# Performance work log

Measured on AMD Instinct MI355X. Metric: run time of the kernel, lower is better.

The kernel has to match this reference:

```python
import jax, jax.numpy as jnp
import numpy as np

N = 100000      # number of nodes/edges
R = 32          # relation_dim
I = 256         # input_dim
O = 256         # output_dim


def setup_inputs() -> dict:
    key = jax.random.key(0)
    k1, k2, k3, k4 = jax.random.split(key, 4)
    x = jax.random.normal(k1, (N, I), dtype=jnp.float32)
    # relation weights per node (e.g. soft relation assignment), non-negative
    edge_attr = jax.random.uniform(k2, (N, R), dtype=jnp.float32)
    # xavier_uniform-style init for W [R, O, I] and b [R, O]
    a_w = float(np.sqrt(6.0 / (I + O)))
    W = jax.random.uniform(k3, (R, O, I), dtype=jnp.float32, minval=-a_w, maxval=a_w)
    a_b = float(np.sqrt(6.0 / (R + O)))
    b = jax.random.uniform(k4, (R, O), dtype=jnp.float32, minval=-a_b, maxval=a_b)
    return {"x": x, "edge_attr": edge_attr, "W": W, "b": b}


def reference(x, edge_attr, W, b):
    # y[n,o] = sum_r edge_attr[n,r] * (W[r] @ x[n])[o] + (edge_attr @ b)[n,o]
    # Stream over the small relation axis, accumulating into [N, O];
    # avoids materializing the naive [N, R, O] intermediate.
    def body(acc, s):
        W_r, e_r = s                      # W_r: [O, I], e_r: [N]
        acc = acc + e_r[:, None] * (x @ W_r.T)  # [N, O]
        return acc, None

    y0 = edge_attr @ b                    # bias term: [N, R] @ [R, O] -> [N, O]
    y, _ = jax.lax.scan(body, y0, (W, edge_attr.T))
    return y
```

## Files before the change

kernel.cpp:

```cpp
#include <hip/hip_runtime.h>
#include <hip/hip_bf16.h>


typedef __attribute__((ext_vector_type(4))) float f32x4;
typedef __attribute__((ext_vector_type(8))) short short8;
typedef __attribute__((ext_vector_type(8))) unsigned short ushort8;

#define R_DIM 32
#define I_DIM 256
#define O_DIM 256
#define KW    8192
#define KEXT  8256
#define BM    128
#define BN    256
#define BK    64
#define NT    (KEXT / BK)
#define NTHR  512

__device__ __forceinline__ unsigned short f2bf(float f) {
  unsigned u = __builtin_bit_cast(unsigned, f);
  u += 0x7FFFu + ((u >> 16) & 1u);
  return (unsigned short)(u >> 16);
}

__device__ __forceinline__ unsigned pk2(float a, float b) {
  __hip_bfloat162 h = __float22bfloat162_rn(make_float2(a, b));
  unsigned u;
  __builtin_memcpy(&u, &h, sizeof(u));
  return u;
}

__device__ __forceinline__ void gld_lds16(const void* g, void* l) {
  __builtin_amdgcn_global_load_lds(
      (const __attribute__((address_space(1))) unsigned int*)g,
      (__attribute__((address_space(3))) unsigned int*)l, 16, 0, 0);
}

__global__ void prep_w(const float* __restrict__ W, const float* __restrict__ b,
                       unsigned short* __restrict__ Wb) {
  const int id = blockIdx.x * 256 + threadIdx.x;
  const int o  = id / (KEXT / 4);
  const int k4 = (id - o * (KEXT / 4)) * 4;
  float v[4];
  if (k4 < KW) {
    const int r  = k4 & 31;
    const int ih = (k4 >> 5) & 1;
    const int il = k4 >> 6;
    const int i  = 128 * ih + il;
#pragma unroll
    for (int j = 0; j < 4; ++j)
      v[j] = W[((size_t)((r + j) * O_DIM + o)) * I_DIM + i];
  } else {
    const int kk = k4 - KW;
#pragma unroll
    for (int j = 0; j < 4; ++j)
      v[j] = (kk + j < R_DIM) ? b[(kk + j) * O_DIM + o] : 0.f;
  }
  uint2 pk;
  pk.x = pk2(v[0], v[1]);
  pk.y = pk2(v[2], v[3]);
  *(uint2*)&Wb[(size_t)o * KEXT + k4] = pk;
}

__global__ __launch_bounds__(NTHR)
__attribute__((amdgpu_waves_per_eu(2, 2)))
void lkg2p(
    const float* __restrict__ x, const float* __restrict__ e,
    const unsigned short* __restrict__ Wb, float* __restrict__ out, int Ntot) {
  __shared__ unsigned short Al[2][BM * BK];
  __shared__ unsigned short Bl[3][BN * BK];

  const int tid  = threadIdx.x;
  const int lane = tid & 63;
  const int w    = tid >> 6;
  const int wr   = w >> 2;
  const int wc   = w & 3;
  const int l15  = lane & 15;
  const int sx   = (l15 & 7) << 4;
  const int kb0  = (lane >> 4) << 4;

  const int m0   = (int)blockIdx.x * BM;
  const int srow = tid >> 2;
  const int q    = tid & 3;
  const int ih   = q >> 1;
  const int gr   = min(m0 + srow, Ntot - 1);

  const int bro = lane >> 3;
  const int bch = (lane & 7) ^ bro;

  float er[16];
#pragma unroll
  for (int p = 0; p < 4; ++p) {
    const float4 ev = *(const float4*)&e[(size_t)gr * R_DIM + (q & 1) * 16 + p * 4];
    er[p * 4 + 0] = ev.x; er[p * 4 + 1] = ev.y;
    er[p * 4 + 2] = ev.z; er[p * 4 + 3] = ev.w;
  }
  const float* xrow = x + (size_t)gr * I_DIM + ih * 128;
  const float bx = (ih == 0) ? 1.f : 0.f;

  f32x4 acc[4][4];
#pragma unroll
  for (int a = 0; a < 4; ++a)
#pragma unroll
    for (int c = 0; c < 4; ++c) acc[a][c] = (f32x4){0.f, 0.f, 0.f, 0.f};

  auto issueB4 = [&](unsigned short* Bd, int t2) {
    const size_t k0 = (size_t)t2 * BK;
#pragma unroll
    for (int g = 0; g < 4; ++g)
      gld_lds16(Wb + (size_t)(w * 32 + g * 8 + bro) * KEXT + k0 + bch * 8,
                Bd + (w * 32 + g * 8) * BK);
  };
  auto stageA = [&](unsigned short* Ad, float xs) {
    char* rowp = (char*)(Ad + srow * BK);
    const int sw = (srow & 7) << 4;
    const int qb = q * 32;
    uint4 wv;
    wv.x = pk2(xs * er[0], xs * er[1]);
    wv.y = pk2(xs * er[2], xs * er[3]);
    wv.z = pk2(xs * er[4], xs * er[5]);
    wv.w = pk2(xs * er[6], xs * er[7]);
    *(uint4*)(rowp + ((qb + 0) ^ sw)) = wv;
    uint4 wv2;
    wv2.x = pk2(xs * er[8],  xs * er[9]);
    wv2.y = pk2(xs * er[10], xs * er[11]);
    wv2.z = pk2(xs * er[12], xs * er[13]);
    wv2.w = pk2(xs * er[14], xs * er[15]);
    *(uint4*)(rowp + ((qb + 16) ^ sw)) = wv2;
  };
  auto rdA = [&](const unsigned short* Ab, int ks, int fr) -> short8 {
    const int row = wr * 64 + fr * 16 + l15;
    return *(const short8*)((const char*)Ab + row * 128 + ((ks * 64 + kb0) ^ sx));
  };
  auto rdB = [&](const unsigned short* Bb, int ks, int fc) -> short8 {
    const int row = wc * 64 + fc * 16 + l15;
    return *(const short8*)((const char*)Bb + row * 128 + ((ks * 64 + kb0) ^ sx));
  };

  auto tileF = [&](int t, float xs, int mode, int apar, int cb) {
    const unsigned short* Ac = Al[apar];
    unsigned short*       Aw = Al[apar ^ 1];
    const unsigned short* Bc = Bl[cb];
    unsigned short*       Bw = Bl[cb >= 1 ? cb - 1 : 2];

    short8 af[4], bf[4];

#pragma unroll
    for (int fr = 0; fr < 4; ++fr) af[fr] = rdA(Ac, 0, fr);
#pragma unroll
    for (int fc = 0; fc < 4; ++fc) bf[fc] = rdB(Bc, 0, fc);
    if (mode & 2) issueB4(Bw, t + 2);
    __builtin_amdgcn_s_barrier();
    asm volatile("s_waitcnt lgkmcnt(0)" ::: "memory");
    __builtin_amdgcn_s_setprio(1);
#pragma unroll
    for (int fr = 0; fr < 4; ++fr)
#pragma unroll
      for (int fc = 0; fc < 4; ++fc)
        acc[fr][fc] = __builtin_amdgcn_mfma_f32_16x16x32_bf16(af[fr], bf[fc],
                                                              acc[fr][fc], 0, 0, 0);
    __builtin_amdgcn_s_setprio(0);
    __builtin_amdgcn_s_barrier();

#pragma unroll
    for (int fr = 0; fr < 4; ++fr) af[fr] = rdA(Ac, 1, fr);
#pragma unroll
    for (int fc = 0; fc < 4; ++fc) bf[fc] = rdB(Bc, 1, fc);
    if (mode & 1) stageA(Aw, xs);
    asm volatile("s_waitcnt lgkmcnt(0)" ::: "memory");
    if (mode & 2) {
      asm volatile("s_waitcnt vmcnt(4)" ::: "memory");
    } else {
      asm volatile("s_waitcnt vmcnt(0)" ::: "memory");
    }
    __builtin_amdgcn_s_barrier();
    __builtin_amdgcn_s_setprio(1);
#pragma unroll
    for (int fr = 0; fr < 4; ++fr)
#pragma unroll
      for (int fc = 0; fc < 4; ++fc)
        acc[fr][fc] = __builtin_amdgcn_mfma_f32_16x16x32_bf16(af[fr], bf[fc],
                                                              acc[fr][fc], 0, 0, 0);
    __builtin_amdgcn_s_setprio(0);
    __builtin_amdgcn_s_barrier();
  };

  float4 xv = *(const float4*)xrow;
  stageA(Al[0], xv.x);
  issueB4(Bl[0], 0);
  issueB4(Bl[1], 1);
  asm volatile("s_waitcnt lgkmcnt(0)" ::: "memory");
  asm volatile("s_waitcnt vmcnt(4)" ::: "memory");
  __builtin_amdgcn_s_barrier();

  int cb = 0;
  for (int u = 0; u < 32; ++u) {
    float4 xvn = xv;
    if (u < 31) xvn = *(const float4*)(xrow + (u + 1) * 4);
    const int t0 = u * 4;
    tileF(t0 + 0, xv.y, 3, 0, cb); cb = (cb == 2) ? 0 : cb + 1;
    tileF(t0 + 1, xv.z, 3, 1, cb); cb = (cb == 2) ? 0 : cb + 1;
    tileF(t0 + 2, xv.w, 3, 0, cb); cb = (cb == 2) ? 0 : cb + 1;
    if (u < 31) {
      tileF(t0 + 3, xvn.x, 3, 1, cb);
    } else {
      tileF(t0 + 3, bx, 1, 1, cb);
    }
    cb = (cb == 2) ? 0 : cb + 1;
    xv = xvn;
  }
  tileF(128, 0.f, 0, 0, cb);

#pragma unroll
  for (int fr = 0; fr < 4; ++fr) {
    const int r0 = m0 + wr * 64 + fr * 16 + (lane >> 4) * 4;
#pragma unroll
    for (int j = 0; j < 4; ++j) {
      const int rr = r0 + j;
      if (rr < Ntot) {
#pragma unroll
        for (int fc = 0; fc < 4; ++fc) {
          const int col = wc * 64 + fc * 16 + l15;
          out[(size_t)rr * O_DIM + col] = acc[fr][fc][j];
        }
      }
    }
  }
}

__global__ __launch_bounds__(256) void lkg_fb(
    const float* __restrict__ x, const float* __restrict__ e,
    const float* __restrict__ Wf, const float* __restrict__ bf32,
    float* __restrict__ out, int Ntot) {
  const int FBK = 64;
  const int FNT = (KW + 64) / FBK;
  __shared__ unsigned short Alds[128 * 64];
  __shared__ unsigned short Blds[256 * 64];

  const int tid = threadIdx.x, lane = tid & 63, wid = tid >> 6;
  const int wr = wid >> 1, wc = wid & 1, l15 = lane & 15, lk8 = (lane >> 4) * 8;
  const int m0 = (int)blockIdx.x * 128;
  const int srow = tid >> 1, skq = (tid & 1) * 32;
  const int gr = min(m0 + srow, Ntot - 1);

  f32x4 acc[4][8];
#pragma unroll
  for (int a = 0; a < 4; ++a)
#pragma unroll
    for (int c = 0; c < 8; ++c) acc[a][c] = (f32x4){0.f, 0.f, 0.f, 0.f};

  for (int t = 0; t < FNT; ++t) {
    const int k0 = t * FBK;
    float av[32];
    if (k0 < KW) {
      const int r = k0 >> 8, i0 = k0 & 255;
      const float ev = e[(size_t)gr * R_DIM + r];
#pragma unroll
      for (int p = 0; p < 8; ++p) {
        const float4 xvv = *(const float4*)&x[(size_t)gr * I_DIM + i0 + skq + p * 4];
        av[p * 4 + 0] = xvv.x * ev; av[p * 4 + 1] = xvv.y * ev;
        av[p * 4 + 2] = xvv.z * ev; av[p * 4 + 3] = xvv.w * ev;
      }
    } else {
#pragma unroll
      for (int s2 = 0; s2 < 32; ++s2) {
        const int kk = skq + s2;
        av[s2] = (kk < R_DIM) ? e[(size_t)gr * R_DIM + kk] : 0.f;
      }
    }
    const int bo = tid;
    if (k0 < KW) {
      const int r = k0 >> 8, i0 = k0 & 255;
#pragma unroll
      for (int h = 0; h < 4; ++h) {
        float bv[16];
#pragma unroll
        for (int p = 0; p < 4; ++p) {
          const float4 wv =
              *(const float4*)&Wf[((size_t)(r * O_DIM + bo)) * I_DIM + i0 + h * 16 + p * 4];
          bv[p * 4 + 0] = wv.x; bv[p * 4 + 1] = wv.y;
          bv[p * 4 + 2] = wv.z; bv[p * 4 + 3] = wv.w;
        }
#pragma unroll
        for (int g2 = 0; g2 < 2; ++g2) {
          ushort8 pw;
#pragma unroll
          for (int j = 0; j < 8; ++j) pw[j] = f2bf(bv[g2 * 8 + j]);
          *(ushort8*)&Blds[bo * FBK + h * 16 + g2 * 8] = pw;
        }
      }
    } else {
#pragma unroll
      for (int h = 0; h < 8; ++h) {
        ushort8 pw;
#pragma unroll
        for (int j = 0; j < 8; ++j) {
          const int kk = h * 8 + j;
          pw[j] = (kk < R_DIM) ? f2bf(bf32[kk * O_DIM + bo]) : (unsigned short)0;
        }
        *(ushort8*)&Blds[bo * FBK + h * 8] = pw;
      }
    }
#pragma unroll
    for (int h = 0; h < 4; ++h) {
      ushort8 pw;
#pragma unroll
      for (int j = 0; j < 8; ++j) pw[j] = f2bf(av[h * 8 + j]);
      *(ushort8*)&Alds[srow * FBK + skq + h * 8] = pw;
    }
    __syncthreads();
#pragma unroll
    for (int ks = 0; ks < 2; ++ks) {
      short8 af[4]; short8 bfr[8];
#pragma unroll
      for (int fr = 0; fr < 4; ++fr)
        af[fr] = *(const short8*)&Alds[(wr * 64 + fr * 16 + l15) * FBK + ks * 32 + lk8];
#pragma unroll
      for (int fc = 0; fc < 8; ++fc)
        bfr[fc] = *(const short8*)&Blds[(wc * 128 + fc * 16 + l15) * FBK + ks * 32 + lk8];
#pragma unroll
      for (int fr = 0; fr < 4; ++fr)
#pragma unroll
        for (int fc = 0; fc < 8; ++fc)
          acc[fr][fc] =
              __builtin_amdgcn_mfma_f32_16x16x32_bf16(af[fr], bfr[fc], acc[fr][fc], 0, 0, 0);
    }
    __syncthreads();
  }
#pragma unroll
  for (int fr = 0; fr < 4; ++fr) {
    const int r0 = m0 + wr * 64 + fr * 16 + (lane >> 4) * 4;
#pragma unroll
    for (int fc = 0; fc < 8; ++fc) {
      const int col = wc * 128 + fc * 16 + l15;
#pragma unroll
      for (int j = 0; j < 4; ++j) {
        const int rr = r0 + j;
        if (rr < Ntot) out[(size_t)rr * O_DIM + col] = acc[fr][fc][j];
      }
    }
  }
}

extern "C" void kernel_launch(void* const* d_in, const int* in_sizes, int n_in,
                              void* d_out, int out_size, void* d_ws, size_t ws_size,
                              hipStream_t stream) {
  const float* x = (const float*)d_in[0];
  const float* e = (const float*)d_in[1];
  const float* W = (const float*)d_in[2];
  const float* b = (const float*)d_in[3];
  float* out = (float*)d_out;
  const int Ntot = in_sizes[0] / I_DIM;

  const size_t wb_bytes = (size_t)O_DIM * KEXT * sizeof(unsigned short);
  if (ws_size >= wb_bytes) {
    unsigned short* Wb = (unsigned short*)d_ws;
    prep_w<<<(O_DIM * (KEXT / 4)) / 256, 256, 0, stream>>>(W, b, Wb);
    lkg2p<<<(Ntot + BM - 1) / BM, NTHR, 0, stream>>>(x, e, Wb, out, Ntot);
  } else {
    lkg_fb<<<(Ntot + 127) / 128, 256, 0, stream>>>(x, e, W, b, out, Ntot);
  }
}
```

Before: 607.3 us.

## Split output columns across two blocks with 128-wide N tiles

```diff
diff --git a/kernel.cpp b/kernel.cpp
--- a/kernel.cpp
+++ b/kernel.cpp
@@ -12,7 +12,7 @@
 #define KW    8192
 #define KEXT  8256
 #define BM    128
-#define BN    256
+#define BNB   128
 #define BK    64
 #define NT    (KEXT / BK)
 #define NTHR  512
@@ -63,12 +63,12 @@
 }
 
 __global__ __launch_bounds__(NTHR)
-__attribute__((amdgpu_waves_per_eu(2, 2)))
-void lkg2p(
+__attribute__((amdgpu_waves_per_eu(4)))
+void lkg2b(
     const float* __restrict__ x, const float* __restrict__ e,
     const unsigned short* __restrict__ Wb, float* __restrict__ out, int Ntot) {
   __shared__ unsigned short Al[2][BM * BK];
-  __shared__ unsigned short Bl[3][BN * BK];
+  __shared__ unsigned short Bl[3][BNB * BK];
 
   const int tid  = threadIdx.x;
   const int lane = tid & 63;
@@ -79,7 +79,11 @@
   const int sx   = (l15 & 7) << 4;
   const int kb0  = (lane >> 4) << 4;
 
-  const int m0   = (int)blockIdx.x * BM;
+  const int mi = (int)blockIdx.x >> 1;
+  const int ni = (int)blockIdx.x & 1;
+  const int m0 = mi * BM;
+  const unsigned short* WbN = Wb + (size_t)(ni * BNB) * KEXT;
+
   const int srow = tid >> 2;
   const int q    = tid & 3;
   const int ih   = q >> 1;
@@ -96,20 +100,20 @@
     er[p * 4 + 2] = ev.z; er[p * 4 + 3] = ev.w;
   }
   const float* xrow = x + (size_t)gr * I_DIM + ih * 128;
-  const float bx = (ih == 0) ? 1.f : 0.f;
-
-  f32x4 acc[4][4];
+  const float biasx = (ih == 0) ? 1.f : 0.f;
+
+  f32x4 acc[4][2];
 #pragma unroll
   for (int a = 0; a < 4; ++a)
 #pragma unroll
-    for (int c = 0; c < 4; ++c) acc[a][c] = (f32x4){0.f, 0.f, 0.f, 0.f};
-
-  auto issueB4 = [&](unsigned short* Bd, int t2) {
+    for (int c = 0; c < 2; ++c) acc[a][c] = (f32x4){0.f, 0.f, 0.f, 0.f};
+
+  auto issueB2 = [&](unsigned short* Bd, int t2) {
     const size_t k0 = (size_t)t2 * BK;
 #pragma unroll
-    for (int g = 0; g < 4; ++g)
-      gld_lds16(Wb + (size_t)(w * 32 + g * 8 + bro) * KEXT + k0 + bch * 8,
-                Bd + (w * 32 + g * 8) * BK);
+    for (int g = 0; g < 2; ++g)
+      gld_lds16(WbN + (size_t)(w * 16 + g * 8 + bro) * KEXT + k0 + bch * 8,
+                Bd + (w * 16 + g * 8) * BK);
   };
   auto stageA = [&](unsigned short* Ad, float xs) {
     char* rowp = (char*)(Ad + srow * BK);
@@ -133,7 +137,7 @@
     return *(const short8*)((const char*)Ab + row * 128 + ((ks * 64 + kb0) ^ sx));
   };
   auto rdB = [&](const unsigned short* Bb, int ks, int fc) -> short8 {
-    const int row = wc * 64 + fc * 16 + l15;
+    const int row = wc * 32 + fc * 16 + l15;
     return *(const short8*)((const char*)Bb + row * 128 + ((ks * 64 + kb0) ^ sx));
   };
 
@@ -143,20 +147,20 @@
     const unsigned short* Bc = Bl[cb];
     unsigned short*       Bw = Bl[cb >= 1 ? cb - 1 : 2];
 
-    short8 af[4], bf[4];
+    short8 af[4], bf[2];
 
 #pragma unroll
     for (int fr = 0; fr < 4; ++fr) af[fr] = rdA(Ac, 0, fr);
 #pragma unroll
-    for (int fc = 0; fc < 4; ++fc) bf[fc] = rdB(Bc, 0, fc);
-    if (mode & 2) issueB4(Bw, t + 2);
+    for (int fc = 0; fc < 2; ++fc) bf[fc] = rdB(Bc, 0, fc);
+    if (mode & 2) issueB2(Bw, t + 2);
     __builtin_amdgcn_s_barrier();
     asm volatile("s_waitcnt lgkmcnt(0)" ::: "memory");
     __builtin_amdgcn_s_setprio(1);
 #pragma unroll
     for (int fr = 0; fr < 4; ++fr)
 #pragma unroll
-      for (int fc = 0; fc < 4; ++fc)
+      for (int fc = 0; fc < 2; ++fc)
         acc[fr][fc] = __builtin_amdgcn_mfma_f32_16x16x32_bf16(af[fr], bf[fc],
                                                               acc[fr][fc], 0, 0, 0);
     __builtin_amdgcn_s_setprio(0);
@@ -165,11 +169,11 @@
 #pragma unroll
     for (int fr = 0; fr < 4; ++fr) af[fr] = rdA(Ac, 1, fr);
 #pragma unroll
-    for (int fc = 0; fc < 4; ++fc) bf[fc] = rdB(Bc, 1, fc);
+    for (int fc = 0; fc < 2; ++fc) bf[fc] = rdB(Bc, 1, fc);
     if (mode & 1) stageA(Aw, xs);
     asm volatile("s_waitcnt lgkmcnt(0)" ::: "memory");
     if (mode & 2) {
-      asm volatile("s_waitcnt vmcnt(4)" ::: "memory");
+      asm volatile("s_waitcnt vmcnt(2)" ::: "memory");
     } else {
       asm volatile("s_waitcnt vmcnt(0)" ::: "memory");
     }
@@ -178,7 +182,7 @@
 #pragma unroll
     for (int fr = 0; fr < 4; ++fr)
 #pragma unroll
-      for (int fc = 0; fc < 4; ++fc)
+      for (int fc = 0; fc < 2; ++fc)
         acc[fr][fc] = __builtin_amdgcn_mfma_f32_16x16x32_bf16(af[fr], bf[fc],
                                                               acc[fr][fc], 0, 0, 0);
     __builtin_amdgcn_s_setprio(0);
@@ -187,10 +191,10 @@
 
   float4 xv = *(const float4*)xrow;
   stageA(Al[0], xv.x);
-  issueB4(Bl[0], 0);
-  issueB4(Bl[1], 1);
+  issueB2(Bl[0], 0);
+  issueB2(Bl[1], 1);
   asm volatile("s_waitcnt lgkmcnt(0)" ::: "memory");
-  asm volatile("s_waitcnt vmcnt(4)" ::: "memory");
+  asm volatile("s_waitcnt vmcnt(2)" ::: "memory");
   __builtin_amdgcn_s_barrier();
 
   int cb = 0;
@@ -204,7 +208,7 @@
     if (u < 31) {
       tileF(t0 + 3, xvn.x, 3, 1, cb);
     } else {
-      tileF(t0 + 3, bx, 1, 1, cb);
+      tileF(t0 + 3, biasx, 1, 1, cb);
     }
     cb = (cb == 2) ? 0 : cb + 1;
     xv = xvn;
@@ -219,8 +223,8 @@
       const int rr = r0 + j;
       if (rr < Ntot) {
 #pragma unroll
-        for (int fc = 0; fc < 4; ++fc) {
-          const int col = wc * 64 + fc * 16 + l15;
+        for (int fc = 0; fc < 2; ++fc) {
+          const int col = ni * BNB + wc * 32 + fc * 16 + l15;
           out[(size_t)rr * O_DIM + col] = acc[fr][fc][j];
         }
       }
@@ -356,7 +360,8 @@
   if (ws_size >= wb_bytes) {
     unsigned short* Wb = (unsigned short*)d_ws;
     prep_w<<<(O_DIM * (KEXT / 4)) / 256, 256, 0, stream>>>(W, b, Wb);
-    lkg2p<<<(Ntot + BM - 1) / BM, NTHR, 0, stream>>>(x, e, Wb, out, Ntot);
+    const int nb = ((Ntot + BM - 1) / BM) * 2;
+    lkg2b<<<nb, NTHR, 0, stream>>>(x, e, Wb, out, Ntot);
   } else {
     lkg_fb<<<(Ntot + 127) / 128, 256, 0, stream>>>(x, e, W, b, out, Ntot);
   }
```

Measured after the change: 519.6 us. 1.17x faster.

## Split output columns across two blocks with 256-thread 128x128 tiles

Applied to the files above, without the earlier changes.

```diff
diff --git a/kernel.cpp b/kernel.cpp
--- a/kernel.cpp
+++ b/kernel.cpp
@@ -12,10 +12,10 @@
 #define KW    8192
 #define KEXT  8256
 #define BM    128
-#define BN    256
+#define BNB   128
 #define BK    64
 #define NT    (KEXT / BK)
-#define NTHR  512
+#define NTHR  256
 
 __device__ __forceinline__ unsigned short f2bf(float f) {
   unsigned u = __builtin_bit_cast(unsigned, f);
@@ -63,40 +63,43 @@
 }
 
 __global__ __launch_bounds__(NTHR)
-__attribute__((amdgpu_waves_per_eu(2, 2)))
-void lkg2p(
+__attribute__((amdgpu_waves_per_eu(2)))
+void lkg64(
     const float* __restrict__ x, const float* __restrict__ e,
     const unsigned short* __restrict__ Wb, float* __restrict__ out, int Ntot) {
   __shared__ unsigned short Al[2][BM * BK];
-  __shared__ unsigned short Bl[3][BN * BK];
+  __shared__ unsigned short Bl[3][BNB * BK];
 
   const int tid  = threadIdx.x;
   const int lane = tid & 63;
   const int w    = tid >> 6;
-  const int wr   = w >> 2;
-  const int wc   = w & 3;
+  const int wr   = w >> 1;
+  const int wc   = w & 1;
   const int l15  = lane & 15;
   const int sx   = (l15 & 7) << 4;
   const int kb0  = (lane >> 4) << 4;
 
-  const int m0   = (int)blockIdx.x * BM;
-  const int srow = tid >> 2;
-  const int q    = tid & 3;
-  const int ih   = q >> 1;
+  const int mi = (int)blockIdx.x >> 1;
+  const int ni = (int)blockIdx.x & 1;
+  const int m0 = mi * BM;
+  const unsigned short* WbN = Wb + (size_t)(ni * BNB) * KEXT;
+
+  const int srow = tid >> 1;
+  const int half = tid & 1;
   const int gr   = min(m0 + srow, Ntot - 1);
 
   const int bro = lane >> 3;
   const int bch = (lane & 7) ^ bro;
 
-  float er[16];
-#pragma unroll
-  for (int p = 0; p < 4; ++p) {
-    const float4 ev = *(const float4*)&e[(size_t)gr * R_DIM + (q & 1) * 16 + p * 4];
+  float er[32];
+#pragma unroll
+  for (int p = 0; p < 8; ++p) {
+    const float4 ev = *(const float4*)&e[(size_t)gr * R_DIM + p * 4];
     er[p * 4 + 0] = ev.x; er[p * 4 + 1] = ev.y;
     er[p * 4 + 2] = ev.z; er[p * 4 + 3] = ev.w;
   }
-  const float* xrow = x + (size_t)gr * I_DIM + ih * 128;
-  const float bx = (ih == 0) ? 1.f : 0.f;
+  const float* xrow = x + (size_t)gr * I_DIM + half * 128;
+  const float biasx = (half == 0) ? 1.f : 0.f;
 
   f32x4 acc[4][4];
 #pragma unroll
@@ -108,25 +111,21 @@
     const size_t k0 = (size_t)t2 * BK;
 #pragma unroll
     for (int g = 0; g < 4; ++g)
-      gld_lds16(Wb + (size_t)(w * 32 + g * 8 + bro) * KEXT + k0 + bch * 8,
+      gld_lds16(WbN + (size_t)(w * 32 + g * 8 + bro) * KEXT + k0 + bch * 8,
                 Bd + (w * 32 + g * 8) * BK);
   };
   auto stageA = [&](unsigned short* Ad, float xs) {
     char* rowp = (char*)(Ad + srow * BK);
     const int sw = (srow & 7) << 4;
-    const int qb = q * 32;
-    uint4 wv;
-    wv.x = pk2(xs * er[0], xs * er[1]);
-    wv.y = pk2(xs * er[2], xs * er[3]);
-    wv.z = pk2(xs * er[4], xs * er[5]);
-    wv.w = pk2(xs * er[6], xs * er[7]);
-    *(uint4*)(rowp + ((qb + 0) ^ sw)) = wv;
-    uint4 wv2;
-    wv2.x = pk2(xs * er[8],  xs * er[9]);
-    wv2.y = pk2(xs * er[10], xs * er[11]);
-    wv2.z = pk2(xs * er[12], xs * er[13]);
-    wv2.w = pk2(xs * er[14], xs * er[15]);
-    *(uint4*)(rowp + ((qb + 16) ^ sw)) = wv2;
+#pragma unroll
+    for (int p = 0; p < 4; ++p) {
+      uint4 wv;
+      wv.x = pk2(xs * er[p * 8 + 0], xs * er[p * 8 + 1]);
+      wv.y = pk2(xs * er[p * 8 + 2], xs * er[p * 8 + 3]);
+      wv.z = pk2(xs * er[p * 8 + 4], xs * er[p * 8 + 5]);
+      wv.w = pk2(xs * er[p * 8 + 6], xs * er[p * 8 + 7]);
+      *(uint4*)(rowp + ((half * 64 + p * 16) ^ sw)) = wv;
+    }
   };
   auto rdA = [&](const unsigned short* Ab, int ks, int fr) -> short8 {
     const int row = wr * 64 + fr * 16 + l15;
@@ -204,7 +203,7 @@
     if (u < 31) {
       tileF(t0 + 3, xvn.x, 3, 1, cb);
     } else {
-      tileF(t0 + 3, bx, 1, 1, cb);
+      tileF(t0 + 3, biasx, 1, 1, cb);
     }
     cb = (cb == 2) ? 0 : cb + 1;
     xv = xvn;
@@ -220,7 +219,7 @@
       if (rr < Ntot) {
 #pragma unroll
         for (int fc = 0; fc < 4; ++fc) {
-          const int col = wc * 64 + fc * 16 + l15;
+          const int col = ni * BNB + wc * 64 + fc * 16 + l15;
           out[(size_t)rr * O_DIM + col] = acc[fr][fc][j];
         }
       }
@@ -356,7 +355,8 @@
   if (ws_size >= wb_bytes) {
     unsigned short* Wb = (unsigned short*)d_ws;
     prep_w<<<(O_DIM * (KEXT / 4)) / 256, 256, 0, stream>>>(W, b, Wb);
-    lkg2p<<<(Ntot + BM - 1) / BM, NTHR, 0, stream>>>(x, e, Wb, out, Ntot);
+    const int nb = ((Ntot + BM - 1) / BM) * 2;
+    lkg64<<<nb, NTHR, 0, stream>>>(x, e, Wb, out, Ntot);
   } else {
     lkg_fb<<<(Ntot + 127) / 128, 256, 0, stream>>>(x, e, W, b, out, Ntot);
   }
```

Result: slower. 1.070 ms (+76.2%).
